# Kernel tuning notes

Hardware: AMD Instinct MI355X
Metric: run time of the kernel (lower is better)

The kernel has to match this reference:

```python
import jax, jax.numpy as jnp
import numpy as np

B, D, W, H = 512, 128, 256, 256  # batch, drive_num, window_size, hidden_size


def setup_inputs() -> dict:
    key = jax.random.key(0)
    k = jax.random.split(key, 7)
    x = jax.random.normal(k[0], (B, D, W), jnp.float32)
    # encode_attn: Linear(window_size + 2*hidden_size, 1)
    attn_w = jax.random.normal(k[1], (W + 2 * H,), jnp.float32) * 0.02
    attn_b = jax.random.normal(k[2], (), jnp.float32) * 0.02
    # single-layer LSTM, input_size=D, hidden_size=H; PyTorch gate order i,f,g,o
    W_ih = jax.random.normal(k[3], (4 * H, D), jnp.float32) * 0.05
    W_hh = jax.random.normal(k[4], (4 * H, H), jnp.float32) * 0.05
    b_ih = jax.random.normal(k[5], (4 * H,), jnp.float32) * 0.05
    b_hh = jax.random.normal(k[6], (4 * H,), jnp.float32) * 0.05
    return {"x": x, "attn_w": attn_w, "attn_b": attn_b,
            "W_ih": W_ih, "W_hh": W_hh, "b_ih": b_ih, "b_hh": b_hh}


def reference(x, attn_w, attn_b, W_ih, W_hh, b_ih, b_hh):
    # x: [B, D, W]
    h_dim = W_hh.shape[1]
    w_h = attn_w[:h_dim]           # weight on repeated hidden state
    w_c = attn_w[h_dim:2 * h_dim]  # weight on repeated cell state
    w_x = attn_w[2 * h_dim:]       # weight on full input row (constant over t)
    # precompute input contribution to attention logits: [B, D]
    e_x = jnp.einsum('bdw,w->bd', x, w_x) + attn_b
    x_steps = jnp.moveaxis(x, 2, 0)  # [W, B, D]

    def step(carry, x_t):
        h, c = carry  # [B, H] each
        # attention logit: h/c terms broadcast over drive dim
        e = e_x + (h @ w_h + c @ w_c)[:, None]  # [B, D]
        a = jax.nn.softmax(e, axis=-1)
        x_hat = a * x_t  # [B, D]
        gates = x_hat @ W_ih.T + b_ih + h @ W_hh.T + b_hh  # [B, 4H]
        i, f, g, o = jnp.split(gates, 4, axis=-1)
        c_new = jax.nn.sigmoid(f) * c + jax.nn.sigmoid(i) * jnp.tanh(g)
        h_new = jax.nn.sigmoid(o) * jnp.tanh(c_new)
        return (h_new, c_new), h_new

    bsz = x.shape[0]
    h0 = jnp.zeros((bsz, h_dim), x.dtype)
    c0 = jnp.zeros((bsz, h_dim), x.dtype)
    _, hs = jax.lax.scan(step, (h0, c0), x_steps)  # hs: [W, B, H]
    return jnp.transpose(hs, (1, 0, 2))  # [B, W, H] == hidden_states[:, 1:]
```

## Files before the change

kernel.cpp:

```cpp
#include <hip/hip_runtime.h>
#include <cstdint>

#define NB 512
#define ND 128
#define NW 256
#define NH 256
#define PGRP 32
#define QGRP 8
#define SLOTS 8
#define SENT32 0x7C007C00u
#define SENT64 0x7C007C007C007C00ull

typedef _Float16 f16;
typedef _Float16 h8 __attribute__((ext_vector_type(8)));
typedef float f32x4 __attribute__((ext_vector_type(4)));
typedef unsigned long long u64;

__device__ __forceinline__ float sigm(float v){ return 1.f/(1.f+__expf(-v)); }
__device__ __forceinline__ float tanh_fast(float v){
  v = fminf(fmaxf(v,-15.f),15.f);
  float e = __expf(2.f*v);
  return (e-1.f)/(e+1.f);
}

__global__ __launch_bounds__(128) void attn_kernel(
    const float* __restrict__ x, const float* __restrict__ attn_w,
    const float* __restrict__ attn_b, float* __restrict__ a_buf)
{
    __shared__ float wx[NW];
    __shared__ float sred[2];
    const int b = blockIdx.x;
    const int d = threadIdx.x;

    wx[d]       = attn_w[2 * NH + d];
    wx[d + 128] = attn_w[2 * NH + d + 128];
    __syncthreads();

    const float4* xr = (const float4*)(x + ((size_t)b * ND + d) * NW);
    float acc = 0.f;
    #pragma unroll 8
    for (int w4 = 0; w4 < NW / 4; ++w4) {
        float4 v = xr[w4];
        acc += v.x * wx[w4*4+0] + v.y * wx[w4*4+1]
             + v.z * wx[w4*4+2] + v.w * wx[w4*4+3];
    }
    float e = acc + attn_b[0];

    float mx = e;
    #pragma unroll
    for (int o = 32; o > 0; o >>= 1) mx = fmaxf(mx, __shfl_xor(mx, o));
    if ((d & 63) == 0) sred[d >> 6] = mx;
    __syncthreads();
    mx = fmaxf(sred[0], sred[1]);
    __syncthreads();

    float p = __expf(e - mx);
    float s = p;
    #pragma unroll
    for (int o = 32; o > 0; o >>= 1) s += __shfl_xor(s, o);
    if ((d & 63) == 0) sred[d >> 6] = s;
    __syncthreads();
    s = sred[0] + sred[1];

    a_buf[(size_t)b * ND + d] = p / s;
}

__global__ __launch_bounds__(512) void pack_kernel(
    const float* __restrict__ W_ih, const float* __restrict__ W_hh,
    const float* __restrict__ b_ih, const float* __restrict__ b_hh,
    f16* __restrict__ Wfrag, float* __restrict__ bias)
{
    int flat = blockIdx.x * 512 + threadIdx.x;
    int l    = flat & 63;
    int kt   = (flat >> 6) % 12;
    int wq   = (flat >> 6) / 12;
    int col16 = l & 15, kb = l >> 4;
    int hcol = (wq >> 3) * 32 + (wq & 7) * 4 + (col16 >> 2);
    int gate = col16 & 3;
    int n    = gate * 256 + hcol;
    int k0   = kt * 32 + kb * 8;

    f16 tmp[8];
    #pragma unroll
    for (int e = 0; e < 8; ++e) {
        int k = k0 + e;
        float v = (k < NH) ? W_hh[(size_t)n * NH + k]
                           : W_ih[(size_t)n * ND + (k - NH)];
        tmp[e] = (f16)v;
    }
    *(h8*)(Wfrag + (size_t)flat * 8) = *(const h8*)tmp;

    if (flat < 1024) bias[flat] = b_ih[flat] + b_hh[flat];
}

__global__ __launch_bounds__(512) void poison_kernel(uint4* __restrict__ hx4)
{
    uint4 v = {SENT32, SENT32, SENT32, SENT32};
    hx4[(size_t)blockIdx.x * 512 + threadIdx.x] = v;
}

__global__ __launch_bounds__(512, 2) void lstm_kernel(
    const float* __restrict__ x, const float* __restrict__ a_buf,
    const float* __restrict__ bias, const f16* __restrict__ Wfrag,
    f16* __restrict__ hx, float* __restrict__ out)
{
    __shared__ __align__(16) unsigned char A16[16 * 768];
    __shared__ float scr[8][272];

    const int tid = threadIdx.x;
    const int w = tid >> 6, l = tid & 63;
    const int p = blockIdx.x & 31, q = blockIdx.x >> 5;

    h8 bfrag[12];
    {
        const h8* wsrc = (const h8*)Wfrag + ((q * 8 + w) * 12) * 64 + l;
        #pragma unroll
        for (int kt = 0; kt < 12; ++kt) bfrag[kt] = wsrc[kt * 64];
    }

    const int m = l >> 2, hh = l & 3;
    const int jcol = q * 32 + w * 4 + hh;
    float bias4[4];
    #pragma unroll
    for (int g = 0; g < 4; ++g) bias4[g] = bias[g * 256 + jcol];
    float cstate = 0.f;

    float areg[8];
    const float* xbase = nullptr;
    const int xrow = tid >> 4, xdc = tid & 15;
    if (tid < 256) {
        int b = p * 16 + xrow;
        #pragma unroll
        for (int e = 0; e < 8; ++e) areg[e] = a_buf[b * ND + xdc * 8 + e];
        xbase = x + ((size_t)b * ND + xdc * 8) * NW;
    }
    const int r2 = tid >> 5, kc = tid & 31;
    const int arow = l & 15, akb = l >> 4;
    const int pr = tid >> 3, pc = tid & 7;

    float4 xq[8];

    {
        int byte = r2 * 768 + kc * 16;
        byte ^= (r2 & 7) << 4;
        h8 z = {};
        *(h8*)(A16 + byte) = z;
    }
    if (tid < 256) {
        #pragma unroll
        for (int e = 0; e < 8; ++e)
            xq[e] = *(const float4*)(xbase + (size_t)e * NW);
        f16 xv[8];
        #pragma unroll
        for (int e = 0; e < 8; ++e) {
            float xf = xq[e].x;
            xq[e] = make_float4(xq[e].y, xq[e].z, xq[e].w, xq[e].x);
            xv[e] = (f16)(xf * areg[e]);
        }
        int byte = xrow * 768 + 512 + xdc * 16;
        byte ^= (xrow & 7) << 4;
        *(h8*)(A16 + byte) = *(const h8*)xv;
    }
    __syncthreads();

    for (int t = 0; t < NW; ++t) {
        f32x4 acc = {0.f, 0.f, 0.f, 0.f};
        #pragma unroll
        for (int kt = 8; kt < 12; ++kt) {
            int byte = arow * 768 + kt * 64 + akb * 16;
            byte ^= (arow & 7) << 4;
            h8 afrag = *(const h8*)(A16 + byte);
            acc = __builtin_amdgcn_mfma_f32_16x16x32_f16(afrag, bfrag[kt], acc, 0, 0, 0);
        }

        if (t > 0) {
            const u64* hrow = (const u64*)
                (hx + ((size_t)((t - 1) & 7) * NB + p * 16 + r2) * NH);
            u64 d0, d1;
            for (;;) {
                d0 = __hip_atomic_load(hrow + kc * 2 + 0,
                        __ATOMIC_RELAXED, __HIP_MEMORY_SCOPE_AGENT);
                d1 = __hip_atomic_load(hrow + kc * 2 + 1,
                        __ATOMIC_RELAXED, __HIP_MEMORY_SCOPE_AGENT);
                if ((unsigned)d0 != SENT32 && (unsigned)(d0 >> 32) != SENT32 &&
                    (unsigned)d1 != SENT32 && (unsigned)(d1 >> 32) != SENT32) break;
                __builtin_amdgcn_s_sleep(1);
            }
            int byte = r2 * 768 + kc * 16;
            byte ^= (r2 & 7) << 4;
            ((u64*)(A16 + byte))[0] = d0;
            ((u64*)(A16 + byte))[1] = d1;
        }
        __syncthreads();

        #pragma unroll
        for (int kt = 0; kt < 8; ++kt) {
            int byte = arow * 768 + kt * 64 + akb * 16;
            byte ^= (arow & 7) << 4;
            h8 afrag = *(const h8*)(A16 + byte);
            acc = __builtin_amdgcn_mfma_f32_16x16x32_f16(afrag, bfrag[kt], acc, 0, 0, 0);
        }

        float hn;
        {
            float* sw = &scr[w][0];
            int col = l & 15, rb = (l >> 4) * 4;
            sw[(rb + 0) * 17 + col] = acc[0];
            sw[(rb + 1) * 17 + col] = acc[1];
            sw[(rb + 2) * 17 + col] = acc[2];
            sw[(rb + 3) * 17 + col] = acc[3];
            asm volatile("s_waitcnt lgkmcnt(0)" ::: "memory");
            float G0 = sw[m * 17 + hh * 4 + 0] + bias4[0];
            float G1 = sw[m * 17 + hh * 4 + 1] + bias4[1];
            float G2 = sw[m * 17 + hh * 4 + 2] + bias4[2];
            float G3 = sw[m * 17 + hh * 4 + 3] + bias4[3];
            float ig = sigm(G0), fg = sigm(G1);
            float gg = tanh_fast(G2), og = sigm(G3);
            cstate = fg * cstate + ig * gg;
            hn = og * tanh_fast(cstate);
        }

        asm volatile("s_waitcnt vmcnt(0)" ::: "memory");

        {
            f16 hf = (f16)hn;
            unsigned short hb = __builtin_bit_cast(unsigned short, hf);
            int other = __shfl_xor((int)hb, 1);
            if (!(l & 1)) {
                unsigned val = (unsigned)hb | ((unsigned)(unsigned short)other << 16);
                unsigned* dst = (unsigned*)((unsigned short*)hx
                                + ((size_t)(t & 7) * NB + p * 16 + m) * NH + jcol);
                __hip_atomic_store(dst, val, __ATOMIC_RELAXED, __HIP_MEMORY_SCOPE_AGENT);
            }
        }

        out[((size_t)(p * 16 + m) * NW + t) * NH + jcol] = hn;

        if (tid < 128) {
            u64* pb = (u64*)((unsigned short*)hx
                     + ((size_t)((t + 3) & 7) * NB + p * 16 + pr) * NH + q * 32 + pc * 4);
            __hip_atomic_store(pb, SENT64, __ATOMIC_RELAXED, __HIP_MEMORY_SCOPE_AGENT);
        }

        if (tid < 256 && t + 1 < NW) {
            if (((t + 1) & 3) == 0) {
                #pragma unroll
                for (int e = 0; e < 8; ++e)
                    xq[e] = *(const float4*)(xbase + (size_t)e * NW + (t + 1));
            }
            f16 xv[8];
            #pragma unroll
            for (int e = 0; e < 8; ++e) {
                float xf = xq[e].x;
                xq[e] = make_float4(xq[e].y, xq[e].z, xq[e].w, xq[e].x);
                xv[e] = (f16)(xf * areg[e]);
            }
            int byte = xrow * 768 + 512 + xdc * 16;
            byte ^= (xrow & 7) << 4;
            *(h8*)(A16 + byte) = *(const h8*)xv;
        }
        __syncthreads();
    }
}

extern "C" void kernel_launch(void* const* d_in, const int* in_sizes, int n_in,
                              void* d_out, int out_size, void* d_ws, size_t ws_size,
                              hipStream_t stream) {
    (void)in_sizes; (void)n_in; (void)out_size;

    const float* x      = (const float*)d_in[0];
    const float* attn_w = (const float*)d_in[1];
    const float* attn_b = (const float*)d_in[2];
    const float* W_ih   = (const float*)d_in[3];
    const float* W_hh   = (const float*)d_in[4];
    const float* b_ih   = (const float*)d_in[5];
    const float* b_hh   = (const float*)d_in[6];
    float* out = (float*)d_out;

    char* ws = (char*)d_ws;
    float* a_buf = (float*)ws;
    float* bias  = (float*)(ws + 262144);
    f16*   Wfrag = (f16*)(ws + 266240);
    f16*   hx    = (f16*)(ws + 1052672);
    if (ws_size < (size_t)(1052672 + 2097152)) return;

    attn_kernel<<<NB, 128, 0, stream>>>(x, attn_w, attn_b, a_buf);
    pack_kernel<<<96, 512, 0, stream>>>(W_ih, W_hh, b_ih, b_hh, Wfrag, bias);
    poison_kernel<<<256, 512, 0, stream>>>((uint4*)hx);
    lstm_kernel<<<PGRP * QGRP, 512, 0, stream>>>(x, a_buf, bias, Wfrag, hx, out);
}
```

Measured before the change: 818.7 us.

## Split LSTM hidden dimension across block pairs to shrink cross-block exchange

Switches the recurrent kernel from 256 blocks (each owning 32 hidden columns for 16 batch rows) to 64 blocks in pairs, each owning half of the hidden dimension for 16 batch rows. Each block keeps its own half of h locally in LDS and exchanges only the other half with its partner through global memory with sentinel polling. Input-projection weights move to a 128KB dynamic LDS buffer, and the W_hh slices are permuted so the local half comes first. The intent is to cut inter-block synchronisation fan-in and global traffic per step, at the cost of more MFMAs per wave, higher register pressure and far fewer active CUs.

```diff
diff --git a/kernel.cpp b/kernel.cpp
--- a/kernel.cpp
+++ b/kernel.cpp
@@ -5,13 +5,11 @@
 #define ND 128
 #define NW 256
 #define NH 256
-#define PGRP 32
-#define QGRP 8
-#define SLOTS 8
 #define SENT32 0x7C007C00u
 #define SENT64 0x7C007C007C007C00ull
 
 typedef _Float16 f16;
+typedef _Float16 h4 __attribute__((ext_vector_type(4)));
 typedef _Float16 h8 __attribute__((ext_vector_type(8)));
 typedef float f32x4 __attribute__((ext_vector_type(4)));
 typedef unsigned long long u64;
@@ -73,19 +71,21 @@
     int flat = blockIdx.x * 512 + threadIdx.x;
     int l    = flat & 63;
     int kt   = (flat >> 6) % 12;
-    int wq   = (flat >> 6) / 12;
-    int col16 = l & 15, kb = l >> 4;
-    int hcol = (wq >> 3) * 32 + (wq & 7) * 4 + (col16 >> 2);
-    int gate = col16 & 3;
-    int n    = gate * 256 + hcol;
-    int k0   = kt * 32 + kb * 8;
+    int tau  = (flat >> 6) / 12;
+    int H    = tau >> 5;
+    int c2   = (l & 15) >> 2, gate = l & 3;
+    int j    = tau * 4 + c2;
+    int n    = gate * 256 + j;
+    int k0   = kt * 32 + (l >> 4) * 8;
 
     f16 tmp[8];
     #pragma unroll
     for (int e = 0; e < 8; ++e) {
         int k = k0 + e;
-        float v = (k < NH) ? W_hh[(size_t)n * NH + k]
-                           : W_ih[(size_t)n * ND + (k - NH)];
+        float v;
+        if (k < 128)      v = W_hh[(size_t)n * NH + H * 128 + k];
+        else if (k < 256) v = W_hh[(size_t)n * NH + (1 - H) * 128 + (k - 128)];
+        else              v = W_ih[(size_t)n * ND + (k - 256)];
         tmp[e] = (f16)v;
     }
     *(h8*)(Wfrag + (size_t)flat * 8) = *(const h8*)tmp;
@@ -104,163 +104,202 @@
     const float* __restrict__ bias, const f16* __restrict__ Wfrag,
     f16* __restrict__ hx, float* __restrict__ out)
 {
-    __shared__ __align__(16) unsigned char A16[16 * 768];
-    __shared__ float scr[8][272];
+    extern __shared__ __align__(16) char smem[];
+    f16* wx = (f16*)smem;
+    unsigned char* A16 = (unsigned char*)smem + 131072;
+    float* scr = (float*)(smem + 143360);
 
     const int tid = threadIdx.x;
     const int w = tid >> 6, l = tid & 63;
-    const int p = blockIdx.x & 31, q = blockIdx.x >> 5;
-
-    h8 bfrag[12];
+    const int g = blockIdx.x >> 1, H = blockIdx.x & 1;
+    const int b0 = g * 16;
+
+    h8 bh[4][4], bp[4][4];
+    #pragma unroll
+    for (int n = 0; n < 4; ++n) {
+        const int tau = H * 32 + w * 4 + n;
+        const h8* base = (const h8*)Wfrag + (size_t)tau * 12 * 64 + l;
+        #pragma unroll
+        for (int ktl = 0; ktl < 4; ++ktl) bh[n][ktl] = base[ktl * 64];
+        #pragma unroll
+        for (int ktl = 0; ktl < 4; ++ktl) bp[n][ktl] = base[(4 + ktl) * 64];
+        #pragma unroll
+        for (int ktl = 0; ktl < 4; ++ktl) {
+            h8 v = base[(8 + ktl) * 64];
+            *(h8*)(wx + ((size_t)(w * 16 + n * 4 + ktl) * 64 + l) * 8) = v;
+        }
+    }
+
+    const int m = l >> 2, hh = l & 3;
+    float biasv[4][4];
+    #pragma unroll
+    for (int n = 0; n < 4; ++n)
+        #pragma unroll
+        for (int gate = 0; gate < 4; ++gate)
+            biasv[n][gate] = bias[gate * 256 + H * 128 + w * 16 + n * 4 + hh];
+    float cstate[4] = {0.f, 0.f, 0.f, 0.f};
+
+    const int xrow = tid >> 5, xdc2 = tid & 31;
+    const int pr = tid >> 4, pc = tid & 15;
+    const int arow = l & 15, akb = l >> 4;
+
+    float areg[4];
+    const float* xbase = x + ((size_t)(b0 + xrow) * ND + xdc2 * 4) * NW;
+    #pragma unroll
+    for (int e = 0; e < 4; ++e)
+        areg[e] = a_buf[(b0 + xrow) * ND + xdc2 * 4 + e];
+    float4 xq[4];
+
+    #define REG_OFF_U64(slot, half) \
+        ((size_t)(((slot) * 32 + g) * 2 + (half)) * 512)
+
     {
-        const h8* wsrc = (const h8*)Wfrag + ((q * 8 + w) * 12) * 64 + l;
-        #pragma unroll
-        for (int kt = 0; kt < 12; ++kt) bfrag[kt] = wsrc[kt * 64];
-    }
-
-    const int m = l >> 2, hh = l & 3;
-    const int jcol = q * 32 + w * 4 + hh;
-    float bias4[4];
-    #pragma unroll
-    for (int g = 0; g < 4; ++g) bias4[g] = bias[g * 256 + jcol];
-    float cstate = 0.f;
-
-    float areg[8];
-    const float* xbase = nullptr;
-    const int xrow = tid >> 4, xdc = tid & 15;
-    if (tid < 256) {
-        int b = p * 16 + xrow;
-        #pragma unroll
-        for (int e = 0; e < 8; ++e) areg[e] = a_buf[b * ND + xdc * 8 + e];
-        xbase = x + ((size_t)b * ND + xdc * 8) * NW;
-    }
-    const int r2 = tid >> 5, kc = tid & 31;
-    const int arow = l & 15, akb = l >> 4;
-    const int pr = tid >> 3, pc = tid & 7;
-
-    float4 xq[8];
-
-    {
-        int byte = r2 * 768 + kc * 16;
-        byte ^= (r2 & 7) << 4;
+        int byte = (tid >> 5) * 768 + (tid & 31) * 16;
+        byte ^= ((tid >> 5) & 7) << 4;
         h8 z = {};
         *(h8*)(A16 + byte) = z;
     }
-    if (tid < 256) {
-        #pragma unroll
-        for (int e = 0; e < 8; ++e)
-            xq[e] = *(const float4*)(xbase + (size_t)e * NW);
-        f16 xv[8];
-        #pragma unroll
-        for (int e = 0; e < 8; ++e) {
+    #pragma unroll
+    for (int e = 0; e < 4; ++e)
+        xq[e] = *(const float4*)(xbase + (size_t)e * NW);
+    {
+        f16 xv[4];
+        #pragma unroll
+        for (int e = 0; e < 4; ++e) {
             float xf = xq[e].x;
             xq[e] = make_float4(xq[e].y, xq[e].z, xq[e].w, xq[e].x);
             xv[e] = (f16)(xf * areg[e]);
         }
-        int byte = xrow * 768 + 512 + xdc * 16;
+        int byte = xrow * 768 + 512 + xdc2 * 8;
         byte ^= (xrow & 7) << 4;
-        *(h8*)(A16 + byte) = *(const h8*)xv;
+        *(h4*)(A16 + byte) = *(const h4*)xv;
     }
     __syncthreads();
 
     for (int t = 0; t < NW; ++t) {
-        f32x4 acc = {0.f, 0.f, 0.f, 0.f};
-        #pragma unroll
-        for (int kt = 8; kt < 12; ++kt) {
-            int byte = arow * 768 + kt * 64 + akb * 16;
+        u64 d0 = 0, d1 = 0;
+        const u64* src = nullptr;
+        if (tid < 256) {
+            u64* pb = (u64*)hx + REG_OFF_U64((t + 3) & 7, 1 - H) + pr * 32 + pc * 2;
+            __hip_atomic_store(pb + 0, SENT64, __ATOMIC_RELAXED, __HIP_MEMORY_SCOPE_AGENT);
+            __hip_atomic_store(pb + 1, SENT64, __ATOMIC_RELAXED, __HIP_MEMORY_SCOPE_AGENT);
+            if (t > 0) {
+                src = (const u64*)hx + REG_OFF_U64((t - 1) & 7, 1 - H) + pr * 32 + pc * 2;
+                d0 = __hip_atomic_load(src + 0, __ATOMIC_RELAXED, __HIP_MEMORY_SCOPE_AGENT);
+                d1 = __hip_atomic_load(src + 1, __ATOMIC_RELAXED, __HIP_MEMORY_SCOPE_AGENT);
+            }
+        }
+
+        f32x4 acc[4] = {{0.f,0.f,0.f,0.f},{0.f,0.f,0.f,0.f},
+                        {0.f,0.f,0.f,0.f},{0.f,0.f,0.f,0.f}};
+        #pragma unroll
+        for (int ktl = 0; ktl < 4; ++ktl) {
+            int byte = arow * 768 + ktl * 64 + akb * 16;
             byte ^= (arow & 7) << 4;
             h8 afrag = *(const h8*)(A16 + byte);
-            acc = __builtin_amdgcn_mfma_f32_16x16x32_f16(afrag, bfrag[kt], acc, 0, 0, 0);
-        }
-
-        if (t > 0) {
-            const u64* hrow = (const u64*)
-                (hx + ((size_t)((t - 1) & 7) * NB + p * 16 + r2) * NH);
-            u64 d0, d1;
+            #pragma unroll
+            for (int n = 0; n < 4; ++n)
+                acc[n] = __builtin_amdgcn_mfma_f32_16x16x32_f16(afrag, bh[n][ktl], acc[n], 0, 0, 0);
+        }
+        #pragma unroll
+        for (int ktl = 0; ktl < 4; ++ktl) {
+            int byte = arow * 768 + (8 + ktl) * 64 + akb * 16;
+            byte ^= (arow & 7) << 4;
+            h8 afrag = *(const h8*)(A16 + byte);
+            #pragma unroll
+            for (int n = 0; n < 4; ++n) {
+                h8 bx = *(const h8*)(wx + ((size_t)(w * 16 + n * 4 + ktl) * 64 + l) * 8);
+                acc[n] = __builtin_amdgcn_mfma_f32_16x16x32_f16(afrag, bx, acc[n], 0, 0, 0);
+            }
+        }
+
+        if (t > 0 && tid < 256) {
             for (;;) {
-                d0 = __hip_atomic_load(hrow + kc * 2 + 0,
-                        __ATOMIC_RELAXED, __HIP_MEMORY_SCOPE_AGENT);
-                d1 = __hip_atomic_load(hrow + kc * 2 + 1,
-                        __ATOMIC_RELAXED, __HIP_MEMORY_SCOPE_AGENT);
                 if ((unsigned)d0 != SENT32 && (unsigned)(d0 >> 32) != SENT32 &&
                     (unsigned)d1 != SENT32 && (unsigned)(d1 >> 32) != SENT32) break;
-                __builtin_amdgcn_s_sleep(1);
-            }
-            int byte = r2 * 768 + kc * 16;
-            byte ^= (r2 & 7) << 4;
+                __builtin_amdgcn_s_sleep(2);
+                d0 = __hip_atomic_load(src + 0, __ATOMIC_RELAXED, __HIP_MEMORY_SCOPE_AGENT);
+                d1 = __hip_atomic_load(src + 1, __ATOMIC_RELAXED, __HIP_MEMORY_SCOPE_AGENT);
+            }
+            int byte = pr * 768 + 256 + pc * 16;
+            byte ^= (pr & 7) << 4;
             ((u64*)(A16 + byte))[0] = d0;
             ((u64*)(A16 + byte))[1] = d1;
         }
         __syncthreads();
 
         #pragma unroll
-        for (int kt = 0; kt < 8; ++kt) {
-            int byte = arow * 768 + kt * 64 + akb * 16;
+        for (int ktl = 0; ktl < 4; ++ktl) {
+            int byte = arow * 768 + (4 + ktl) * 64 + akb * 16;
             byte ^= (arow & 7) << 4;
             h8 afrag = *(const h8*)(A16 + byte);
-            acc = __builtin_amdgcn_mfma_f32_16x16x32_f16(afrag, bfrag[kt], acc, 0, 0, 0);
-        }
-
-        float hn;
-        {
-            float* sw = &scr[w][0];
-            int col = l & 15, rb = (l >> 4) * 4;
-            sw[(rb + 0) * 17 + col] = acc[0];
-            sw[(rb + 1) * 17 + col] = acc[1];
-            sw[(rb + 2) * 17 + col] = acc[2];
-            sw[(rb + 3) * 17 + col] = acc[3];
+            #pragma unroll
+            for (int n = 0; n < 4; ++n)
+                acc[n] = __builtin_amdgcn_mfma_f32_16x16x32_f16(afrag, bp[n][ktl], acc[n], 0, 0, 0);
+        }
+
+        float hn[4];
+        float* sw = scr + w * 272;
+        const int col = l & 15, rb = (l >> 4) * 4;
+        #pragma unroll
+        for (int n = 0; n < 4; ++n) {
+            sw[(rb + 0) * 17 + col] = acc[n][0];
+            sw[(rb + 1) * 17 + col] = acc[n][1];
+            sw[(rb + 2) * 17 + col] = acc[n][2];
+            sw[(rb + 3) * 17 + col] = acc[n][3];
             asm volatile("s_waitcnt lgkmcnt(0)" ::: "memory");
-            float G0 = sw[m * 17 + hh * 4 + 0] + bias4[0];
-            float G1 = sw[m * 17 + hh * 4 + 1] + bias4[1];
-            float G2 = sw[m * 17 + hh * 4 + 2] + bias4[2];
-            float G3 = sw[m * 17 + hh * 4 + 3] + bias4[3];
+            float G0 = sw[m * 17 + hh * 4 + 0] + biasv[n][0];
+            float G1 = sw[m * 17 + hh * 4 + 1] + biasv[n][1];
+            float G2 = sw[m * 17 + hh * 4 + 2] + biasv[n][2];
+            float G3 = sw[m * 17 + hh * 4 + 3] + biasv[n][3];
             float ig = sigm(G0), fg = sigm(G1);
             float gg = tanh_fast(G2), og = sigm(G3);
-            cstate = fg * cstate + ig * gg;
-            hn = og * tanh_fast(cstate);
-        }
-
-        asm volatile("s_waitcnt vmcnt(0)" ::: "memory");
-
-        {
-            f16 hf = (f16)hn;
+            cstate[n] = fg * cstate[n] + ig * gg;
+            hn[n] = og * tanh_fast(cstate[n]);
+
+            const int jl = w * 16 + n * 4 + hh;
+            {
+                int byte = m * 768 + jl * 2;
+                byte ^= (m & 7) << 4;
+                *(f16*)(A16 + byte) = (f16)hn[n];
+            }
+            f16 hf = (f16)hn[n];
             unsigned short hb = __builtin_bit_cast(unsigned short, hf);
             int other = __shfl_xor((int)hb, 1);
             if (!(l & 1)) {
                 unsigned val = (unsigned)hb | ((unsigned)(unsigned short)other << 16);
-                unsigned* dst = (unsigned*)((unsigned short*)hx
-                                + ((size_t)(t & 7) * NB + p * 16 + m) * NH + jcol);
+                unsigned* dst = (unsigned*)hx + REG_OFF_U64(t & 7, H) * 2
+                              + m * 64 + (jl >> 1);
                 __hip_atomic_store(dst, val, __ATOMIC_RELAXED, __HIP_MEMORY_SCOPE_AGENT);
             }
         }
 
-        out[((size_t)(p * 16 + m) * NW + t) * NH + jcol] = hn;
-
-        if (tid < 128) {
-            u64* pb = (u64*)((unsigned short*)hx
-                     + ((size_t)((t + 3) & 7) * NB + p * 16 + pr) * NH + q * 32 + pc * 4);
-            __hip_atomic_store(pb, SENT64, __ATOMIC_RELAXED, __HIP_MEMORY_SCOPE_AGENT);
-        }
-
-        if (tid < 256 && t + 1 < NW) {
+        asm volatile("s_waitcnt vmcnt(0)" ::: "memory");
+
+        #pragma unroll
+        for (int n = 0; n < 4; ++n)
+            out[((size_t)(b0 + m) * NW + t) * NH + H * 128 + w * 16 + n * 4 + hh] = hn[n];
+
+        if (t + 1 < NW) {
             if (((t + 1) & 3) == 0) {
                 #pragma unroll
-                for (int e = 0; e < 8; ++e)
+                for (int e = 0; e < 4; ++e)
                     xq[e] = *(const float4*)(xbase + (size_t)e * NW + (t + 1));
             }
-            f16 xv[8];
+            f16 xv[4];
             #pragma unroll
-            for (int e = 0; e < 8; ++e) {
+            for (int e = 0; e < 4; ++e) {
                 float xf = xq[e].x;
                 xq[e] = make_float4(xq[e].y, xq[e].z, xq[e].w, xq[e].x);
                 xv[e] = (f16)(xf * areg[e]);
             }
-            int byte = xrow * 768 + 512 + xdc * 16;
+            int byte = xrow * 768 + 512 + xdc2 * 8;
             byte ^= (xrow & 7) << 4;
-            *(h8*)(A16 + byte) = *(const h8*)xv;
+            *(h4*)(A16 + byte) = *(const h4*)xv;
         }
         __syncthreads();
     }
+    #undef REG_OFF_U64
 }
 
 extern "C" void kernel_launch(void* const* d_in, const int* in_sizes, int n_in,
@@ -282,10 +321,14 @@
     float* bias  = (float*)(ws + 262144);
     f16*   Wfrag = (f16*)(ws + 266240);
     f16*   hx    = (f16*)(ws + 1052672);
-    if (ws_size < (size_t)(1052672 + 2097152)) return;
+    if (ws_size < (size_t)3149824) return;
+
+    const int smem_bytes = 152064;
+    hipFuncSetAttribute((const void*)lstm_kernel,
+                        hipFuncAttributeMaxDynamicSharedMemorySize, smem_bytes);
 
     attn_kernel<<<NB, 128, 0, stream>>>(x, attn_w, attn_b, a_buf);
     pack_kernel<<<96, 512, 0, stream>>>(W_ih, W_hh, b_ih, b_hh, Wfrag, bias);
     poison_kernel<<<256, 512, 0, stream>>>((uint4*)hx);
-    lstm_kernel<<<PGRP * QGRP, 512, 0, stream>>>(x, a_buf, bias, Wfrag, hx, out);
-}
+    lstm_kernel<<<64, 512, smem_bytes, stream>>>(x, a_buf, bias, Wfrag, hx, out);
+}
```

After: 1.006 ms. +22.9%, slower.

## Double-buffer LSTM A-tile, skip self-exchange of h, shuffle-based gate gather

Applied to the files above, without the earlier changes.

Double-buffers the shared A tile so each block writes its own new h columns straight into the next step's buffer. Only the other 7 column groups are fetched from the global exchange buffer, and those polling loads are issued early, before the x-part MFMAs, to hide latency. The LDS scratch round-trip for gate regrouping is replaced by cross-lane shuffles, and h stores are widened to 64-bit. Poisoning is spread across one peer group with a different slot distance. This adds register pressure and a subtler protocol for when slots get reset.

```diff
diff --git a/kernel.cpp b/kernel.cpp
--- a/kernel.cpp
+++ b/kernel.cpp
@@ -7,7 +7,6 @@
 #define NH 256
 #define PGRP 32
 #define QGRP 8
-#define SLOTS 8
 #define SENT32 0x7C007C00u
 #define SENT64 0x7C007C007C007C00ull
 
@@ -104,12 +103,12 @@
     const float* __restrict__ bias, const f16* __restrict__ Wfrag,
     f16* __restrict__ hx, float* __restrict__ out)
 {
-    __shared__ __align__(16) unsigned char A16[16 * 768];
-    __shared__ float scr[8][272];
+    __shared__ __align__(16) unsigned char A16[2][16 * 768];
 
     const int tid = threadIdx.x;
     const int w = tid >> 6, l = tid & 63;
     const int p = blockIdx.x & 31, q = blockIdx.x >> 5;
+    const int b0 = p * 16;
 
     h8 bfrag[12];
     {
@@ -118,33 +117,35 @@
         for (int kt = 0; kt < 12; ++kt) bfrag[kt] = wsrc[kt * 64];
     }
 
-    const int m = l >> 2, hh = l & 3;
-    const int jcol = q * 32 + w * 4 + hh;
+    const int erow = 4 * (l >> 4) + (l & 3);
+    const int ehc  = (l & 15) >> 2;
+    const int jcol = q * 32 + w * 4 + ehc;
     float bias4[4];
     #pragma unroll
     for (int g = 0; g < 4; ++g) bias4[g] = bias[g * 256 + jcol];
     float cstate = 0.f;
 
+    const int arow = l & 15, akb = l >> 4;
+    const int xrow = tid >> 4, xdc = tid & 15;
+    const int prow = tid >> 3, pc = tid & 7;
+    const bool pact = (tid < 128) && (pc != q);
+    const bool poisoner = (tid < 128) && (pc == ((q + 1) & 7));
+
     float areg[8];
-    const float* xbase = nullptr;
-    const int xrow = tid >> 4, xdc = tid & 15;
+    const float* xbase = x;
     if (tid < 256) {
-        int b = p * 16 + xrow;
+        int b = b0 + xrow;
         #pragma unroll
         for (int e = 0; e < 8; ++e) areg[e] = a_buf[b * ND + xdc * 8 + e];
         xbase = x + ((size_t)b * ND + xdc * 8) * NW;
     }
-    const int r2 = tid >> 5, kc = tid & 31;
-    const int arow = l & 15, akb = l >> 4;
-    const int pr = tid >> 3, pc = tid & 7;
-
     float4 xq[8];
 
     {
-        int byte = r2 * 768 + kc * 16;
-        byte ^= (r2 & 7) << 4;
+        int byte = (tid >> 5) * 768 + (tid & 31) * 16;
+        byte ^= ((tid >> 5) & 7) << 4;
         h8 z = {};
-        *(h8*)(A16 + byte) = z;
+        *(h8*)(A16[0] + byte) = z;
     }
     if (tid < 256) {
         #pragma unroll
@@ -159,37 +160,59 @@
         }
         int byte = xrow * 768 + 512 + xdc * 16;
         byte ^= (xrow & 7) << 4;
-        *(h8*)(A16 + byte) = *(const h8*)xv;
+        *(h8*)(A16[0] + byte) = *(const h8*)xv;
     }
     __syncthreads();
 
     for (int t = 0; t < NW; ++t) {
+        u64 dv[8];
+        u64* hbase = nullptr;
+        if (t > 0 && pact) {
+            hbase = (u64*)hx + (((size_t)((t - 1) & 7)) * NB + b0 + prow) * 64 + pc * 8;
+            #pragma unroll
+            for (int k = 0; k < 8; ++k)
+                dv[k] = __hip_atomic_load(hbase + k,
+                        __ATOMIC_RELAXED, __HIP_MEMORY_SCOPE_AGENT);
+        }
+
         f32x4 acc = {0.f, 0.f, 0.f, 0.f};
         #pragma unroll
         for (int kt = 8; kt < 12; ++kt) {
             int byte = arow * 768 + kt * 64 + akb * 16;
             byte ^= (arow & 7) << 4;
-            h8 afrag = *(const h8*)(A16 + byte);
+            h8 afrag = *(const h8*)(A16[t & 1] + byte);
             acc = __builtin_amdgcn_mfma_f32_16x16x32_f16(afrag, bfrag[kt], acc, 0, 0, 0);
         }
 
-        if (t > 0) {
-            const u64* hrow = (const u64*)
-                (hx + ((size_t)((t - 1) & 7) * NB + p * 16 + r2) * NH);
-            u64 d0, d1;
+        if (t > 0 && pact) {
             for (;;) {
-                d0 = __hip_atomic_load(hrow + kc * 2 + 0,
-                        __ATOMIC_RELAXED, __HIP_MEMORY_SCOPE_AGENT);
-                d1 = __hip_atomic_load(hrow + kc * 2 + 1,
-                        __ATOMIC_RELAXED, __HIP_MEMORY_SCOPE_AGENT);
-                if ((unsigned)d0 != SENT32 && (unsigned)(d0 >> 32) != SENT32 &&
-                    (unsigned)d1 != SENT32 && (unsigned)(d1 >> 32) != SENT32) break;
+                bool ok = true;
+                #pragma unroll
+                for (int k = 0; k < 8; ++k)
+                    ok = ok && ((unsigned)dv[k] != SENT32)
+                            && ((unsigned)(dv[k] >> 32) != SENT32);
+                if (ok) break;
                 __builtin_amdgcn_s_sleep(1);
-            }
-            int byte = r2 * 768 + kc * 16;
-            byte ^= (r2 & 7) << 4;
-            ((u64*)(A16 + byte))[0] = d0;
-            ((u64*)(A16 + byte))[1] = d1;
+                #pragma unroll
+                for (int k = 0; k < 8; ++k)
+                    dv[k] = __hip_atomic_load(hbase + k,
+                            __ATOMIC_RELAXED, __HIP_MEMORY_SCOPE_AGENT);
+            }
+            int base = prow * 768 + pc * 64;
+            #pragma unroll
+            for (int j = 0; j < 4; ++j) {
+                int ad = (base + j * 16) ^ ((prow & 7) << 4);
+                u64* pp = (u64*)(A16[t & 1] + ad);
+                pp[0] = dv[2 * j];
+                pp[1] = dv[2 * j + 1];
+            }
+            if (poisoner) {
+                u64* pz = (u64*)hx + (((size_t)((t + 6) & 7)) * NB + b0 + prow) * 64 + pc * 8;
+                #pragma unroll
+                for (int k = 0; k < 8; ++k)
+                    __hip_atomic_store(pz + k, SENT64,
+                            __ATOMIC_RELAXED, __HIP_MEMORY_SCOPE_AGENT);
+            }
         }
         __syncthreads();
 
@@ -197,50 +220,42 @@
         for (int kt = 0; kt < 8; ++kt) {
             int byte = arow * 768 + kt * 64 + akb * 16;
             byte ^= (arow & 7) << 4;
-            h8 afrag = *(const h8*)(A16 + byte);
+            h8 afrag = *(const h8*)(A16[t & 1] + byte);
             acc = __builtin_amdgcn_mfma_f32_16x16x32_f16(afrag, bfrag[kt], acc, 0, 0, 0);
         }
 
-        float hn;
+        float v0 = acc[0], v1 = acc[1], v2 = acc[2], v3 = acc[3];
         {
-            float* sw = &scr[w][0];
-            int col = l & 15, rb = (l >> 4) * 4;
-            sw[(rb + 0) * 17 + col] = acc[0];
-            sw[(rb + 1) * 17 + col] = acc[1];
-            sw[(rb + 2) * 17 + col] = acc[2];
-            sw[(rb + 3) * 17 + col] = acc[3];
-            asm volatile("s_waitcnt lgkmcnt(0)" ::: "memory");
-            float G0 = sw[m * 17 + hh * 4 + 0] + bias4[0];
-            float G1 = sw[m * 17 + hh * 4 + 1] + bias4[1];
-            float G2 = sw[m * 17 + hh * 4 + 2] + bias4[2];
-            float G3 = sw[m * 17 + hh * 4 + 3] + bias4[3];
-            float ig = sigm(G0), fg = sigm(G1);
-            float gg = tanh_fast(G2), og = sigm(G3);
-            cstate = fg * cstate + ig * gg;
-            hn = og * tanh_fast(cstate);
-        }
-
-        asm volatile("s_waitcnt vmcnt(0)" ::: "memory");
-
+            float t0 = __shfl_xor((l & 1) ? v0 : v1, 1);
+            float t1 = __shfl_xor((l & 1) ? v2 : v3, 1);
+            if (l & 1) { v0 = t0; v2 = t1; } else { v1 = t0; v3 = t1; }
+            float t2 = __shfl_xor((l & 2) ? v0 : v2, 2);
+            float t3 = __shfl_xor((l & 2) ? v1 : v3, 2);
+            if (l & 2) { v0 = t2; v1 = t3; } else { v2 = t2; v3 = t3; }
+        }
+        float G0 = v0 + bias4[0], G1 = v1 + bias4[1];
+        float G2 = v2 + bias4[2], G3 = v3 + bias4[3];
+        float ig = sigm(G0), fg = sigm(G1);
+        float gg = tanh_fast(G2), og = sigm(G3);
+        cstate = fg * cstate + ig * gg;
+        float hn = og * tanh_fast(cstate);
+
+        f16 hf = (f16)hn;
+        unsigned hb = (unsigned)__builtin_bit_cast(unsigned short, hf);
+        unsigned ph = (unsigned)__shfl_xor((int)hb, 4);
+        unsigned pair = hb | (ph << 16);
+        unsigned hi = (unsigned)__shfl_xor((int)pair, 8);
+        if ((l & 12) == 0) {
+            u64 val = (u64)pair | ((u64)hi << 32);
+            u64* dst = (u64*)hx + (((size_t)(t & 7)) * NB + b0 + erow) * 64 + q * 8 + w;
+            __hip_atomic_store(dst, val, __ATOMIC_RELAXED, __HIP_MEMORY_SCOPE_AGENT);
+        }
         {
-            f16 hf = (f16)hn;
-            unsigned short hb = __builtin_bit_cast(unsigned short, hf);
-            int other = __shfl_xor((int)hb, 1);
-            if (!(l & 1)) {
-                unsigned val = (unsigned)hb | ((unsigned)(unsigned short)other << 16);
-                unsigned* dst = (unsigned*)((unsigned short*)hx
-                                + ((size_t)(t & 7) * NB + p * 16 + m) * NH + jcol);
-                __hip_atomic_store(dst, val, __ATOMIC_RELAXED, __HIP_MEMORY_SCOPE_AGENT);
-            }
-        }
-
-        out[((size_t)(p * 16 + m) * NW + t) * NH + jcol] = hn;
-
-        if (tid < 128) {
-            u64* pb = (u64*)((unsigned short*)hx
-                     + ((size_t)((t + 3) & 7) * NB + p * 16 + pr) * NH + q * 32 + pc * 4);
-            __hip_atomic_store(pb, SENT64, __ATOMIC_RELAXED, __HIP_MEMORY_SCOPE_AGENT);
-        }
+            int byte = erow * 768 + jcol * 2;
+            byte ^= (erow & 7) << 4;
+            *(f16*)(A16[(t + 1) & 1] + byte) = hf;
+        }
+        out[((size_t)(b0 + erow) * NW + t) * NH + jcol] = hn;
 
         if (tid < 256 && t + 1 < NW) {
             if (((t + 1) & 3) == 0) {
@@ -257,8 +272,10 @@
             }
             int byte = xrow * 768 + 512 + xdc * 16;
             byte ^= (xrow & 7) << 4;
-            *(h8*)(A16 + byte) = *(const h8*)xv;
-        }
+            *(h8*)(A16[(t + 1) & 1] + byte) = *(const h8*)xv;
+        }
+
+        asm volatile("s_waitcnt vmcnt(0)" ::: "memory");
         __syncthreads();
     }
 }
@@ -282,7 +299,7 @@
     float* bias  = (float*)(ws + 262144);
     f16*   Wfrag = (f16*)(ws + 266240);
     f16*   hx    = (f16*)(ws + 1052672);
-    if (ws_size < (size_t)(1052672 + 2097152)) return;
+    if (ws_size < (size_t)3149824) return;
 
     attn_kernel<<<NB, 128, 0, stream>>>(x, attn_w, attn_b, a_buf);
     pack_kernel<<<96, 512, 0, stream>>>(W_ih, W_hh, b_ih, b_hh, Wfrag, bias);
```

After: 2.418 ms. 195% more time.

## Shrink hidden-state ring to 4 slots, double-buffer LDS, and issue h loads early

Applied to the files above, without the earlier changes.

Cuts the global hidden-state exchange ring from 8 to 4 slots. Hidden-state loads for the previous step are now issued before the x-part MFMAs so their latency overlaps compute, and the LDS A tile is double-buffered so the next x slice can be written while the current one is read. Sentinel re-poisoning of a future slot moves to one q-group per step, rotating over q, with full 512-thread stores, and the vmcnt wait before the h store is removed. The shorter ring with a t+2 poison distance tightens the margin against slow blocks and could risk a race if blocks drift too far apart.

```diff
diff --git a/kernel.cpp b/kernel.cpp
--- a/kernel.cpp
+++ b/kernel.cpp
@@ -7,7 +7,7 @@
 #define NH 256
 #define PGRP 32
 #define QGRP 8
-#define SLOTS 8
+#define SLOTS 4
 #define SENT32 0x7C007C00u
 #define SENT64 0x7C007C007C007C00ull
 
@@ -104,12 +104,13 @@
     const float* __restrict__ bias, const f16* __restrict__ Wfrag,
     f16* __restrict__ hx, float* __restrict__ out)
 {
-    __shared__ __align__(16) unsigned char A16[16 * 768];
+    __shared__ __align__(16) unsigned char A16[2][16 * 768];
     __shared__ float scr[8][272];
 
     const int tid = threadIdx.x;
     const int w = tid >> 6, l = tid & 63;
     const int p = blockIdx.x & 31, q = blockIdx.x >> 5;
+    const int b0 = p * 16;
 
     h8 bfrag[12];
     {
@@ -125,26 +126,25 @@
     for (int g = 0; g < 4; ++g) bias4[g] = bias[g * 256 + jcol];
     float cstate = 0.f;
 
+    const int xrow = tid >> 4, xdc = tid & 15;
+    const int r2 = tid >> 5, kc = tid & 31;
+    const int arow = l & 15, akb = l >> 4;
+
     float areg[8];
-    const float* xbase = nullptr;
-    const int xrow = tid >> 4, xdc = tid & 15;
+    const float* xbase = x;
     if (tid < 256) {
-        int b = p * 16 + xrow;
+        int b = b0 + xrow;
         #pragma unroll
         for (int e = 0; e < 8; ++e) areg[e] = a_buf[b * ND + xdc * 8 + e];
         xbase = x + ((size_t)b * ND + xdc * 8) * NW;
     }
-    const int r2 = tid >> 5, kc = tid & 31;
-    const int arow = l & 15, akb = l >> 4;
-    const int pr = tid >> 3, pc = tid & 7;
-
     float4 xq[8];
 
     {
         int byte = r2 * 768 + kc * 16;
         byte ^= (r2 & 7) << 4;
         h8 z = {};
-        *(h8*)(A16 + byte) = z;
+        *(h8*)(A16[0] + byte) = z;
     }
     if (tid < 256) {
         #pragma unroll
@@ -159,45 +159,56 @@
         }
         int byte = xrow * 768 + 512 + xdc * 16;
         byte ^= (xrow & 7) << 4;
-        *(h8*)(A16 + byte) = *(const h8*)xv;
+        *(h8*)(A16[0] + byte) = *(const h8*)xv;
     }
     __syncthreads();
 
     for (int t = 0; t < NW; ++t) {
+        u64 d0 = 0, d1 = 0;
+        const u64* src = nullptr;
+        if (t > 0) {
+            src = (const u64*)hx
+                + (((size_t)((t - 1) & 3)) * NB + b0 + r2) * 64 + kc * 2;
+            d0 = __hip_atomic_load(src + 0, __ATOMIC_RELAXED, __HIP_MEMORY_SCOPE_AGENT);
+            d1 = __hip_atomic_load(src + 1, __ATOMIC_RELAXED, __HIP_MEMORY_SCOPE_AGENT);
+        }
+
         f32x4 acc = {0.f, 0.f, 0.f, 0.f};
         #pragma unroll
         for (int kt = 8; kt < 12; ++kt) {
             int byte = arow * 768 + kt * 64 + akb * 16;
             byte ^= (arow & 7) << 4;
-            h8 afrag = *(const h8*)(A16 + byte);
+            h8 afrag = *(const h8*)(A16[t & 1] + byte);
             acc = __builtin_amdgcn_mfma_f32_16x16x32_f16(afrag, bfrag[kt], acc, 0, 0, 0);
         }
 
         if (t > 0) {
-            const u64* hrow = (const u64*)
-                (hx + ((size_t)((t - 1) & 7) * NB + p * 16 + r2) * NH);
-            u64 d0, d1;
             for (;;) {
-                d0 = __hip_atomic_load(hrow + kc * 2 + 0,
-                        __ATOMIC_RELAXED, __HIP_MEMORY_SCOPE_AGENT);
-                d1 = __hip_atomic_load(hrow + kc * 2 + 1,
-                        __ATOMIC_RELAXED, __HIP_MEMORY_SCOPE_AGENT);
                 if ((unsigned)d0 != SENT32 && (unsigned)(d0 >> 32) != SENT32 &&
                     (unsigned)d1 != SENT32 && (unsigned)(d1 >> 32) != SENT32) break;
                 __builtin_amdgcn_s_sleep(1);
+                d0 = __hip_atomic_load(src + 0, __ATOMIC_RELAXED, __HIP_MEMORY_SCOPE_AGENT);
+                d1 = __hip_atomic_load(src + 1, __ATOMIC_RELAXED, __HIP_MEMORY_SCOPE_AGENT);
             }
             int byte = r2 * 768 + kc * 16;
             byte ^= (r2 & 7) << 4;
-            ((u64*)(A16 + byte))[0] = d0;
-            ((u64*)(A16 + byte))[1] = d1;
+            ((u64*)(A16[t & 1] + byte))[0] = d0;
+            ((u64*)(A16[t & 1] + byte))[1] = d1;
         }
         __syncthreads();
+
+        if (q == (t & 7)) {
+            u64* pz = (u64*)hx
+                + (((size_t)((t + 2) & 3)) * NB + b0 + r2) * 64 + kc * 2;
+            __hip_atomic_store(pz + 0, SENT64, __ATOMIC_RELAXED, __HIP_MEMORY_SCOPE_AGENT);
+            __hip_atomic_store(pz + 1, SENT64, __ATOMIC_RELAXED, __HIP_MEMORY_SCOPE_AGENT);
+        }
 
         #pragma unroll
         for (int kt = 0; kt < 8; ++kt) {
             int byte = arow * 768 + kt * 64 + akb * 16;
             byte ^= (arow & 7) << 4;
-            h8 afrag = *(const h8*)(A16 + byte);
+            h8 afrag = *(const h8*)(A16[t & 1] + byte);
             acc = __builtin_amdgcn_mfma_f32_16x16x32_f16(afrag, bfrag[kt], acc, 0, 0, 0);
         }
 
@@ -218,29 +229,19 @@
             float gg = tanh_fast(G2), og = sigm(G3);
             cstate = fg * cstate + ig * gg;
             hn = og * tanh_fast(cstate);
-        }
-
-        asm volatile("s_waitcnt vmcnt(0)" ::: "memory");
-
-        {
+
             f16 hf = (f16)hn;
             unsigned short hb = __builtin_bit_cast(unsigned short, hf);
             int other = __shfl_xor((int)hb, 1);
             if (!(l & 1)) {
                 unsigned val = (unsigned)hb | ((unsigned)(unsigned short)other << 16);
                 unsigned* dst = (unsigned*)((unsigned short*)hx
-                                + ((size_t)(t & 7) * NB + p * 16 + m) * NH + jcol);
+                                + ((size_t)(t & 3) * NB + b0 + m) * NH + jcol);
                 __hip_atomic_store(dst, val, __ATOMIC_RELAXED, __HIP_MEMORY_SCOPE_AGENT);
             }
         }
 
-        out[((size_t)(p * 16 + m) * NW + t) * NH + jcol] = hn;
-
-        if (tid < 128) {
-            u64* pb = (u64*)((unsigned short*)hx
-                     + ((size_t)((t + 3) & 7) * NB + p * 16 + pr) * NH + q * 32 + pc * 4);
-            __hip_atomic_store(pb, SENT64, __ATOMIC_RELAXED, __HIP_MEMORY_SCOPE_AGENT);
-        }
+        out[((size_t)(b0 + m) * NW + t) * NH + jcol] = hn;
 
         if (tid < 256 && t + 1 < NW) {
             if (((t + 1) & 3) == 0) {
@@ -257,7 +258,7 @@
             }
             int byte = xrow * 768 + 512 + xdc * 16;
             byte ^= (xrow & 7) << 4;
-            *(h8*)(A16 + byte) = *(const h8*)xv;
+            *(h8*)(A16[(t + 1) & 1] + byte) = *(const h8*)xv;
         }
         __syncthreads();
     }
@@ -282,10 +283,10 @@
     float* bias  = (float*)(ws + 262144);
     f16*   Wfrag = (f16*)(ws + 266240);
     f16*   hx    = (f16*)(ws + 1052672);
-    if (ws_size < (size_t)(1052672 + 2097152)) return;
+    if (ws_size < (size_t)2101248) return;
 
     attn_kernel<<<NB, 128, 0, stream>>>(x, attn_w, attn_b, a_buf);
     pack_kernel<<<96, 512, 0, stream>>>(W_ih, W_hh, b_ih, b_hh, Wfrag, bias);
-    poison_kernel<<<256, 512, 0, stream>>>((uint4*)hx);
+    poison_kernel<<<128, 512, 0, stream>>>((uint4*)hx);
     lstm_kernel<<<PGRP * QGRP, 512, 0, stream>>>(x, a_buf, bias, Wfrag, hx, out);
 }
```

New measurement: 1.990 ms. 2.43x slower.
